# Optimization experiments

Measured on AMD Instinct MI355X. Metric: run time of the kernel, lower is better.

Reference implementation:

```python
import jax, jax.numpy as jnp
import numpy as np

# Rs_hidden = [(16,0),(16,1)] -> 16 scalar irreps (dim 1) then 16 vector irreps (dim 3)
B, N, M = 4, 80, 16
CH = M + 3 * M  # 64 channels
RADII = jnp.linspace(0.0, 1.0, 3)
GAMMA = 1.0 / (0.5 ** 2)  # gaussian rbf width = radii spacing
EPS = 1e-6

_lc = np.zeros((3, 3, 3), np.float32)
for i, j, k in [(0, 1, 2), (1, 2, 0), (2, 0, 1)]:
    _lc[i, j, k] = 1.0
    _lc[i, k, j] = -1.0
LC = jnp.asarray(_lc)  # Levi-Civita


def _si(t, w0, w1):
    """SelfInteraction: per-l mixing of multiplicities. t: [B, mi0 + 3*mi1, ...]."""
    mi0, mi1 = w0.shape[1], w1.shape[1]
    s = t[:, :mi0]
    v = t[:, mi0:].reshape(t.shape[0], mi1, 3, *t.shape[2:])
    os = jnp.einsum('om,nm...->no...', w0, s)
    ov = jnp.einsum('om,nmi...->noi...', w1, v)
    ov = ov.reshape(ov.shape[0], ov.shape[1] * 3, *ov.shape[3:])
    return jnp.concatenate([os, ov], axis=1)


def _norm_act(t, act):
    """NormActivation: scalar irreps -> act(x); vector irreps -> x * act(||x||)/||x||. Channel axis 1."""
    s = act(t[:, :M])
    v = t[:, M:].reshape(t.shape[0], M, 3, *t.shape[2:])
    n = jnp.sqrt(jnp.sum(v * v, axis=2, keepdims=True) + EPS)
    v = (v * act(n) / n).reshape(t.shape[0], 3 * M, *t.shape[2:])
    return jnp.concatenate([s, v], axis=1)


def _gate_mul(gate, target):
    """gate_normwise_multiply: multiply each irrep block of target by the L2 norm of the
    corresponding gate block (norm over the irrep components, channel axis 1)."""
    gs = jnp.abs(gate[:, :M])
    gv = gate[:, M:].reshape(gate.shape[0], M, 3, *gate.shape[2:])
    gn = jnp.sqrt(jnp.sum(gv * gv, axis=2) + EPS)
    factor = jnp.concatenate([gs, jnp.repeat(gn, 3, axis=1)], axis=1)
    return factor * target


def _interleave(a_t, b_t):
    """Interleave per-(m,l) blocks: [a_l0, b_l0, a_l1, b_l1] -> Rs_hidden_double layout."""
    return jnp.concatenate([a_t[:, :M], b_t[:, :M], a_t[:, M:], b_t[:, M:]], axis=1)


def _kernel(h_nei_diff, w_k00, w_k10, w_k01, w_k11):
    """SE3 point kernel for l in {0,1}, J<=2. Returns K[n,b,a,d,c] with d,c in irrep layout."""
    rad = jnp.sqrt(jnp.sum(h_nei_diff ** 2, axis=-1) + EPS)      # [B,N,N]
    nh = h_nei_diff / rad[..., None]                              # unit vectors
    rbf = jnp.exp(-GAMMA * (rad[..., None] - RADII) ** 2)        # [B,N,N,3]
    K00 = jnp.einsum('uvk,...k->...uv', w_k00, rbf)              # [B,N,N,M,M]
    K10 = jnp.einsum('uvk,...k,...i->...uiv', w_k10, rbf, nh).reshape(B, N, N, 3 * M, M)
    K01 = jnp.einsum('uvk,...k,...j->...uvj', w_k01, rbf, nh).reshape(B, N, N, M, 3 * M)
    RJ = jnp.einsum('juvk,...k->j...uv', w_k11, rbf)             # [3,B,N,N,M,M]
    eye = jnp.eye(3, dtype=rbf.dtype)
    cross = jnp.einsum('ijk,...k->...ij', LC, nh)                # J=1 basis
    outer = nh[..., :, None] * nh[..., None, :] - eye / 3.0      # J=2 basis
    base = (RJ[0][..., None, None] * eye
            + RJ[1][..., None, None] * cross[..., None, None, :, :]
            + RJ[2][..., None, None] * outer[..., None, None, :, :])  # [B,N,N,u,v,i,j]
    K11 = jnp.transpose(base, (0, 1, 2, 3, 5, 4, 6)).reshape(B, N, N, 3 * M, 3 * M)
    top = jnp.concatenate([K00, K01], axis=-1)
    bot = jnp.concatenate([K10, K11], axis=-1)
    return jnp.concatenate([top, bot], axis=-2)                  # [B,N,N,CH,CH]


def setup_inputs() -> dict:
    key = jax.random.key(0)
    ks = jax.random.split(key, 16)
    sc = 0.1
    d = {
        'x': jax.random.normal(ks[0], (B, CH, N), jnp.float32),
        'h_nei': jax.random.normal(ks[1], (B, CH, N), jnp.float32),
        'h_nei_diff': jax.random.normal(ks[2], (B, N, N, 3), jnp.float32),
        'mask': jax.random.uniform(ks[3], (B, N, N), jnp.float32),
        'w_k00': jax.random.normal(ks[4], (M, M, 3), jnp.float32) * sc,
        'w_k10': jax.random.normal(ks[5], (M, M, 3), jnp.float32) * sc,
        'w_k01': jax.random.normal(ks[6], (M, M, 3), jnp.float32) * sc,
        'w_k11': jax.random.normal(ks[7], (3, M, M, 3), jnp.float32) * sc,
        'si_z_w0': jax.random.normal(ks[8], (M, 2 * M), jnp.float32) * sc,
        'si_z_w1': jax.random.normal(ks[9], (M, 2 * M), jnp.float32) * sc,
        'si_r1_w0': jax.random.normal(ks[10], (M, M), jnp.float32) * sc,
        'si_r1_w1': jax.random.normal(ks[11], (M, M), jnp.float32) * sc,
        'si_r2_w0': jax.random.normal(ks[12], (M, M), jnp.float32) * sc,
        'si_r2_w1': jax.random.normal(ks[13], (M, M), jnp.float32) * sc,
        'si_ph_w0': jax.random.normal(ks[14], (M, 2 * M), jnp.float32) * sc,
        'si_ph_w1': jax.random.normal(ks[15], (M, 2 * M), jnp.float32) * sc,
    }
    return d


def reference(x, h_nei, h_nei_diff, mask, w_k00, w_k10, w_k01, w_k11,
              si_z_w0, si_z_w1, si_r1_w0, si_r1_w1, si_r2_w0, si_r2_w1,
              si_ph_w0, si_ph_w1):
    Kmat = _kernel(h_nei_diff, w_k00, w_k10, w_k01, w_k11)
    # masked neighbor conv: h_conv[n,d,b,a] = sum_c h_nei[n,c,a] K[n,b,a,d,c] mask[n,b,a]
    h_conv = jnp.einsum('nca,nbadc,nba->ndba', h_nei, Kmat, mask)
    sum_h = h_conv.sum(axis=-1)                                   # [B,CH,N]
    z = _norm_act(_si(_interleave(x, sum_h), si_z_w0, si_z_w1), jax.nn.sigmoid)
    r1 = _si(x, si_r1_w0, si_r1_w1)                               # [B,CH,N]
    r2 = _si(h_conv.reshape(B, CH, N * N), si_r2_w0, si_r2_w1).reshape(B, CH, N, N)
    r = _norm_act(r1[:, :, None, :] + r2, jax.nn.sigmoid)         # [B,CH,N,N]
    gated = _gate_mul(r, h_conv)
    sum_g = gated.sum(axis=-1)                                    # [B,CH,N]
    pre_h = _norm_act(_si(_interleave(x, sum_g), si_ph_w0, si_ph_w1), jnp.tanh)
    new_h = sum_h + _gate_mul(z, pre_h + sum_h)
    return new_h
```

## Files before the change

### kernel.cpp

```cpp
#include <hip/hip_runtime.h>
#include <math.h>

#define Bq 4
#define Nq 80
#define CHq 64
#define GAMMAq 4.0f
#define EPSq 1e-6f
#define PCWL 100
#define NQUAD 24


__global__ __launch_bounds__(64) void se3_precomp(
    const float* __restrict__ h_nei,
    const float* __restrict__ x,
    const float* __restrict__ w00,
    const float* __restrict__ w10,
    const float* __restrict__ w01,
    const float* __restrict__ w11,
    const float* __restrict__ wr10,
    const float* __restrict__ wr11,
    const float* __restrict__ wr20,
    const float* __restrict__ wr21,
    float* __restrict__ pc)
{
    const int na = blockIdx.x;
    const int n  = na / Nq, a = na - n * Nq;
    const int t  = threadIdx.x;
    const int u  = t & 15;
    const int kk = t >> 4;

    __shared__ float hsh[64];
    __shared__ float xsh[64];
    __shared__ float pout[16][PCWL];

    hsh[t] = h_nei[(size_t)n * CHq * Nq + t * Nq + a];
    xsh[t] = x    [(size_t)n * CHq * Nq + t * Nq + a];
    __syncthreads();

    if (kk < 3) {
        const int k = kk;
        float a00 = 0.f, a10 = 0.f;
        float c[3] = {0.f,0.f,0.f}, p0[3] = {0.f,0.f,0.f};
        float p1[3] = {0.f,0.f,0.f}, p2[3] = {0.f,0.f,0.f};
#pragma unroll
        for (int v = 0; v < 16; ++v) {
            const float s = hsh[v];
            a00 += w00[(u * 16 + v) * 3 + k] * s;
            a10 += w10[(u * 16 + v) * 3 + k] * s;
            const float w01v = w01[(u * 16 + v) * 3 + k];
            const float w110 = w11[((0 * 16 + u) * 16 + v) * 3 + k];
            const float w111 = w11[((1 * 16 + u) * 16 + v) * 3 + k];
            const float w112 = w11[((2 * 16 + u) * 16 + v) * 3 + k];
#pragma unroll
            for (int j = 0; j < 3; ++j) {
                const float Vj = hsh[16 + v * 3 + j];
                c[j]  += w01v * Vj;
                p0[j] += w110 * Vj;
                p1[j] += w111 * Vj;
                p2[j] += w112 * Vj;
            }
        }
        pout[u][0 + k] = a00;
        pout[u][3 + k] = a10;
#pragma unroll
        for (int j = 0; j < 3; ++j) {
            pout[u][6  + k * 3 + j] = c[j];
            pout[u][15 + k * 3 + j] = p0[j];
            pout[u][24 + k * 3 + j] = p1[j];
            pout[u][33 + k * 3 + j] = p2[j];
        }
    } else {
        float r1s = 0.f, r1v[3] = {0.f, 0.f, 0.f};
#pragma unroll
        for (int v = 0; v < 16; ++v) {
            r1s += wr10[u * 16 + v] * xsh[v];
            const float wv = wr11[u * 16 + v];
#pragma unroll
            for (int j = 0; j < 3; ++j) r1v[j] += wv * xsh[16 + v * 3 + j];
        }
        pout[u][42] = r1s;
#pragma unroll
        for (int j = 0; j < 3; ++j) pout[u][43 + j] = r1v[j];
        pout[u][46] = 0.f; pout[u][47] = 0.f;
#pragma unroll
        for (int j = 90; j < 96; ++j) pout[u][j] = 0.f;
    }
    __syncthreads();

    for (int c = kk; c < 42; c += 4) {
        const bool scalarType = (c < 3) || (c >= 6 && c < 15);
        const float* W = scalarType ? wr20 : wr21;
        float acc = 0.f;
#pragma unroll
        for (int v = 0; v < 16; ++v) acc += W[u * 16 + v] * pout[v][c];
        pout[u][48 + c] = acc;
    }
    __syncthreads();

    {
        float4* dst = reinterpret_cast<float4*>(pc) + (size_t)na * (NQUAD * 16) + u;
#pragma unroll
        for (int i = 0; i < 6; ++i) {
            const int c4 = kk + i * 4;
            dst[c4 * 16] = make_float4(pout[u][c4 * 4 + 0], pout[u][c4 * 4 + 1],
                                       pout[u][c4 * 4 + 2], pout[u][c4 * 4 + 3]);
        }
    }
}

__global__ __launch_bounds__(256) void se3_main(
    const float* __restrict__ x,
    const float* __restrict__ hdiff,
    const float* __restrict__ mask,
    const float* __restrict__ wz0,
    const float* __restrict__ wz1,
    const float* __restrict__ wp0,
    const float* __restrict__ wp1,
    const float* __restrict__ pc,
    float* __restrict__ out)
{
    const int nb    = blockIdx.x;
    const int n     = nb / Nq;
    const int bnode = nb - n * Nq;
    const int tid   = threadIdx.x;
    const int g     = tid >> 4;
    const int u     = tid & 15;

    __shared__ float wsh[4][512];
    __shared__ float redW[4][8][16];
    __shared__ float sumHs[64], sumGs[64];

#pragma unroll
    for (int i = 0; i < 2; ++i) {
        const int idx = tid + i * 256;
        wsh[0][idx] = wz0[idx];
        wsh[1][idx] = wz1[idx];
        wsh[2][idx] = wp0[idx];
        wsh[3][idx] = wp1[idx];
    }

    float shs = 0.f, shv0 = 0.f, shv1 = 0.f, shv2 = 0.f;
    float sgs = 0.f, sgv0 = 0.f, sgv1 = 0.f, sgv2 = 0.f;

    const float* drow = hdiff + (size_t)(n * Nq + bnode) * Nq * 3;
    const float* mrow = mask  + (size_t)(n * Nq + bnode) * Nq;
    const float third = 1.0f / 3.0f;

    for (int it = 0; it < 5; ++it) {
        const int a = it * 16 + g;

        const float d0 = drow[a * 3 + 0], d1 = drow[a * 3 + 1], d2 = drow[a * 3 + 2];
        const float m  = mrow[a];

        const float rad = sqrtf(d0 * d0 + d1 * d1 + d2 * d2 + EPSq);
        const float inv = 1.0f / rad;
        const float nh0 = d0 * inv, nh1 = d1 * inv, nh2 = d2 * inv;
        float rb[3];
        rb[0] = expf(-GAMMAq * rad * rad);
        { float t1 = rad - 0.5f; rb[1] = expf(-GAMMAq * t1 * t1); }
        { float t2 = rad - 1.0f; rb[2] = expf(-GAMMAq * t2 * t2); }

        const float4* p4 = reinterpret_cast<const float4*>(pc)
                         + (size_t)(n * Nq + a) * (NQUAD * 16) + u;

        float pa[48];
#pragma unroll
        for (int i = 0; i < 12; ++i)
            *reinterpret_cast<float4*>(&pa[i * 4]) = p4[i * 16];
        float pb[44];
#pragma unroll
        for (int i = 0; i < 11; ++i)
            *reinterpret_cast<float4*>(&pb[i * 4]) = p4[(12 + i) * 16];

        float as_ = 0.f, a10 = 0.f;
        float c01[3] = {0.f,0.f,0.f}, p0[3] = {0.f,0.f,0.f};
        float p1[3] = {0.f,0.f,0.f}, p2[3] = {0.f,0.f,0.f};
        float bs_ = 0.f, b10 = 0.f;
        float bc01[3] = {0.f,0.f,0.f}, bp0[3] = {0.f,0.f,0.f};
        float bp1[3] = {0.f,0.f,0.f}, bp2[3] = {0.f,0.f,0.f};
#pragma unroll
        for (int k = 0; k < 3; ++k) {
            const float r = rb[k];
            as_ += r * pa[0 + k];
            a10 += r * pa[3 + k];
            bs_ += r * pb[0 + k];
            b10 += r * pb[3 + k];
#pragma unroll
            for (int j = 0; j < 3; ++j) {
                c01[j]  += r * pa[6  + k * 3 + j];
                p0[j]   += r * pa[15 + k * 3 + j];
                p1[j]   += r * pa[24 + k * 3 + j];
                p2[j]   += r * pa[33 + k * 3 + j];
                bc01[j] += r * pb[6  + k * 3 + j];
                bp0[j]  += r * pb[15 + k * 3 + j];
                bp1[j]  += r * pb[24 + k * 3 + j];
                bp2[j]  += r * pb[33 + k * 3 + j];
            }
        }

        const float hcs = m * (as_ + c01[0] * nh0 + c01[1] * nh1 + c01[2] * nh2);
        const float cr0 = p1[1] * nh2 - p1[2] * nh1;
        const float cr1 = p1[2] * nh0 - p1[0] * nh2;
        const float cr2 = p1[0] * nh1 - p1[1] * nh0;
        const float pd  = p2[0] * nh0 + p2[1] * nh1 + p2[2] * nh2;
        const float hv0 = m * (nh0 * a10 + p0[0] + cr0 + nh0 * pd - p2[0] * third);
        const float hv1 = m * (nh1 * a10 + p0[1] + cr1 + nh1 * pd - p2[1] * third);
        const float hv2 = m * (nh2 * a10 + p0[2] + cr2 + nh2 * pd - p2[2] * third);

        const float r2s = m * (bs_ + bc01[0] * nh0 + bc01[1] * nh1 + bc01[2] * nh2);
        const float br0 = bp1[1] * nh2 - bp1[2] * nh1;
        const float br1 = bp1[2] * nh0 - bp1[0] * nh2;
        const float br2 = bp1[0] * nh1 - bp1[1] * nh0;
        const float bpd = bp2[0] * nh0 + bp2[1] * nh1 + bp2[2] * nh2;
        const float r2v0 = m * (nh0 * b10 + bp0[0] + br0 + nh0 * bpd - bp2[0] * third);
        const float r2v1 = m * (nh1 * b10 + bp0[1] + br1 + nh1 * bpd - bp2[1] * third);
        const float r2v2 = m * (nh2 * b10 + bp0[2] + br2 + nh2 * bpd - bp2[2] * third);

        const float r1s  = pa[42];
        const float r1v0 = pa[43], r1v1 = pa[44], r1v2 = pa[45];

        const float rs  = 1.0f / (1.0f + expf(-(r1s + r2s)));
        const float wv0 = r1v0 + r2v0, wv1 = r1v1 + r2v1, wv2 = r1v2 + r2v2;
        const float nn  = sqrtf(wv0 * wv0 + wv1 * wv1 + wv2 * wv2 + EPSq);
        const float sc  = (1.0f / (1.0f + expf(-nn))) / nn;
        const float rv0 = wv0 * sc, rv1 = wv1 * sc, rv2 = wv2 * sc;
        const float fs  = fabsf(rs);
        const float fv  = sqrtf(rv0 * rv0 + rv1 * rv1 + rv2 * rv2 + EPSq);

        shs += hcs;        shv0 += hv0;      shv1 += hv1;      shv2 += hv2;
        sgs += fs * hcs;   sgv0 += fv * hv0; sgv1 += fv * hv1; sgv2 += fv * hv2;
    }

    float vals[8] = {shs, shv0, shv1, shv2, sgs, sgv0, sgv1, sgv2};
#pragma unroll
    for (int q = 0; q < 8; ++q) {
        vals[q] += __shfl_xor(vals[q], 16, 64);
        vals[q] += __shfl_xor(vals[q], 32, 64);
    }
    const int wave = tid >> 6;
    if ((tid & 63) < 16) {
#pragma unroll
        for (int q = 0; q < 8; ++q) redW[wave][q][u] = vals[q];
    }
    __syncthreads();

    if (tid < 16) {
        float tacc[8];
#pragma unroll
        for (int q = 0; q < 8; ++q)
            tacc[q] = redW[0][q][tid] + redW[1][q][tid] + redW[2][q][tid] + redW[3][q][tid];
        sumHs[tid] = tacc[0];
        sumGs[tid] = tacc[4];
#pragma unroll
        for (int j = 0; j < 3; ++j) {
            sumHs[16 + tid * 3 + j] = tacc[1 + j];
            sumGs[16 + tid * 3 + j] = tacc[5 + j];
        }
    }
    __syncthreads();

    if (tid < 16) {
        const float* xb = x + (size_t)n * CHq * Nq + bnode;

        float zs_in = 0.f, ps_in = 0.f;
        float zv[3] = {0.f, 0.f, 0.f};
        float pv[3] = {0.f, 0.f, 0.f};
#pragma unroll
        for (int mm = 0; mm < 32; ++mm) {
            float Sh, Sg;
            if (mm < 16) { const float xv = xb[mm * Nq]; Sh = xv; Sg = xv; }
            else         { Sh = sumHs[mm - 16]; Sg = sumGs[mm - 16]; }
            zs_in += wsh[0][tid * 32 + mm] * Sh;
            ps_in += wsh[2][tid * 32 + mm] * Sg;
            const float wz = wsh[1][tid * 32 + mm];
            const float wp = wsh[3][tid * 32 + mm];
#pragma unroll
            for (int j = 0; j < 3; ++j) {
                float Vh, Vg;
                if (mm < 16) { const float xv = xb[(16 + mm * 3 + j) * Nq]; Vh = xv; Vg = xv; }
                else { Vh = sumHs[16 + (mm - 16) * 3 + j]; Vg = sumGs[16 + (mm - 16) * 3 + j]; }
                zv[j] += wz * Vh;
                pv[j] += wp * Vg;
            }
        }

        const float zs  = 1.0f / (1.0f + expf(-zs_in));
        const float zn  = sqrtf(zv[0] * zv[0] + zv[1] * zv[1] + zv[2] * zv[2] + EPSq);
        const float zsc = (1.0f / (1.0f + expf(-zn))) / zn;
        const float zv0 = zv[0] * zsc, zv1 = zv[1] * zsc, zv2 = zv[2] * zsc;
        const float phs = tanhf(ps_in);
        const float pn  = sqrtf(pv[0] * pv[0] + pv[1] * pv[1] + pv[2] * pv[2] + EPSq);
        const float psc = tanhf(pn) / pn;
        const float pv0 = pv[0] * psc, pv1 = pv[1] * psc, pv2 = pv[2] * psc;
        const float gfs = fabsf(zs);
        const float gfv = sqrtf(zv0 * zv0 + zv1 * zv1 + zv2 * zv2 + EPSq);

        float* ob = out + (size_t)n * CHq * Nq + bnode;
        const float sh_s = sumHs[tid];
        ob[tid * Nq] = sh_s + gfs * (phs + sh_s);
#pragma unroll
        for (int j = 0; j < 3; ++j) {
            const float shv = sumHs[16 + tid * 3 + j];
            const float pvj = (j == 0) ? pv0 : ((j == 1) ? pv1 : pv2);
            ob[(16 + tid * 3 + j) * Nq] = shv + gfv * (pvj + shv);
        }
    }
}

extern "C" void kernel_launch(void* const* d_in, const int* in_sizes, int n_in,
                              void* d_out, int out_size, void* d_ws, size_t ws_size,
                              hipStream_t stream) {
    const float* x      = (const float*)d_in[0];
    const float* h_nei  = (const float*)d_in[1];
    const float* hdiff  = (const float*)d_in[2];
    const float* mask   = (const float*)d_in[3];
    const float* w00    = (const float*)d_in[4];
    const float* w10    = (const float*)d_in[5];
    const float* w01    = (const float*)d_in[6];
    const float* w11    = (const float*)d_in[7];
    const float* wz0    = (const float*)d_in[8];
    const float* wz1    = (const float*)d_in[9];
    const float* wr10   = (const float*)d_in[10];
    const float* wr11   = (const float*)d_in[11];
    const float* wr20   = (const float*)d_in[12];
    const float* wr21   = (const float*)d_in[13];
    const float* wp0    = (const float*)d_in[14];
    const float* wp1    = (const float*)d_in[15];
    float* out = (float*)d_out;
    float* pc  = (float*)d_ws;

    se3_precomp<<<Bq * Nq, 64, 0, stream>>>(
        h_nei, x, w00, w10, w01, w11, wr10, wr11, wr20, wr21, pc);
    se3_main<<<Bq * Nq, 256, 0, stream>>>(
        x, hdiff, mask, wz0, wz1, wp0, wp1, pc, out);
}
```

Baseline: 27.69 us.

## Split precompute reductions across more threads, remap block indices, use fast exp

The precompute kernel grows from 64 to 192 threads. Each v-reduction is split into two halves whose partial sums are combined in shared memory, and the second-stage r2 mixing is spread over 96 threads instead of 64. Both kernels remap blockIdx so that consecutive blocks alternate across batch and node halves, likely to spread work across XCDs and their caches. expf is replaced by __expf in the main kernel, trading a little accuracy for cheaper transcendentals.

```diff
diff --git a/kernel.cpp b/kernel.cpp
--- a/kernel.cpp
+++ b/kernel.cpp
@@ -10,7 +10,7 @@
 #define NQUAD 24
 
 
-__global__ __launch_bounds__(64) void se3_precomp(
+__global__ __launch_bounds__(192) void se3_precomp(
     const float* __restrict__ h_nei,
     const float* __restrict__ x,
     const float* __restrict__ w00,
@@ -23,87 +23,121 @@
     const float* __restrict__ wr21,
     float* __restrict__ pc)
 {
-    const int na = blockIdx.x;
-    const int n  = na / Nq, a = na - n * Nq;
-    const int t  = threadIdx.x;
-    const int u  = t & 15;
-    const int kk = t >> 4;
+    const int L   = blockIdx.x & 7;
+    const int idx = blockIdx.x >> 3;
+    const int n   = L >> 1;
+    const int a   = (L & 1) * 40 + idx;
+    const int na  = n * Nq + a;
+    const int tid = threadIdx.x;
 
     __shared__ float hsh[64];
     __shared__ float xsh[64];
+    __shared__ float psh[2][42][16];
+    __shared__ float r1sh[2][4][16];
     __shared__ float pout[16][PCWL];
 
-    hsh[t] = h_nei[(size_t)n * CHq * Nq + t * Nq + a];
-    xsh[t] = x    [(size_t)n * CHq * Nq + t * Nq + a];
-    __syncthreads();
-
-    if (kk < 3) {
-        const int k = kk;
-        float a00 = 0.f, a10 = 0.f;
-        float c[3] = {0.f,0.f,0.f}, p0[3] = {0.f,0.f,0.f};
-        float p1[3] = {0.f,0.f,0.f}, p2[3] = {0.f,0.f,0.f};
-#pragma unroll
-        for (int v = 0; v < 16; ++v) {
-            const float s = hsh[v];
-            a00 += w00[(u * 16 + v) * 3 + k] * s;
-            a10 += w10[(u * 16 + v) * 3 + k] * s;
-            const float w01v = w01[(u * 16 + v) * 3 + k];
-            const float w110 = w11[((0 * 16 + u) * 16 + v) * 3 + k];
-            const float w111 = w11[((1 * 16 + u) * 16 + v) * 3 + k];
-            const float w112 = w11[((2 * 16 + u) * 16 + v) * 3 + k];
+    if (tid < 64)       hsh[tid]      = h_nei[(size_t)n * CHq * Nq + tid * Nq + a];
+    else if (tid < 128) xsh[tid - 64] = x    [(size_t)n * CHq * Nq + (tid - 64) * Nq + a];
+    __syncthreads();
+
+    if (tid < 128) {
+        const int u    = tid & 15;
+        const int q    = tid >> 4;
+        const int half = q & 1;
+        const int kk   = q >> 1;
+        const int v0   = half * 8;
+
+        if (kk < 3) {
+            const int k = kk;
+            float a00 = 0.f, a10 = 0.f;
+            float c[3] = {0.f,0.f,0.f}, p0[3] = {0.f,0.f,0.f};
+            float p1[3] = {0.f,0.f,0.f}, p2[3] = {0.f,0.f,0.f};
+#pragma unroll
+            for (int i = 0; i < 8; ++i) {
+                const int v = v0 + i;
+                const float s = hsh[v];
+                a00 += w00[(u * 16 + v) * 3 + k] * s;
+                a10 += w10[(u * 16 + v) * 3 + k] * s;
+                const float w01v = w01[(u * 16 + v) * 3 + k];
+                const float w110 = w11[((0 * 16 + u) * 16 + v) * 3 + k];
+                const float w111 = w11[((1 * 16 + u) * 16 + v) * 3 + k];
+                const float w112 = w11[((2 * 16 + u) * 16 + v) * 3 + k];
+#pragma unroll
+                for (int j = 0; j < 3; ++j) {
+                    const float Vj = hsh[16 + v * 3 + j];
+                    c[j]  += w01v * Vj;
+                    p0[j] += w110 * Vj;
+                    p1[j] += w111 * Vj;
+                    p2[j] += w112 * Vj;
+                }
+            }
+            psh[half][0 + k][u] = a00;
+            psh[half][3 + k][u] = a10;
 #pragma unroll
             for (int j = 0; j < 3; ++j) {
-                const float Vj = hsh[16 + v * 3 + j];
-                c[j]  += w01v * Vj;
-                p0[j] += w110 * Vj;
-                p1[j] += w111 * Vj;
-                p2[j] += w112 * Vj;
-            }
-        }
-        pout[u][0 + k] = a00;
-        pout[u][3 + k] = a10;
-#pragma unroll
-        for (int j = 0; j < 3; ++j) {
-            pout[u][6  + k * 3 + j] = c[j];
-            pout[u][15 + k * 3 + j] = p0[j];
-            pout[u][24 + k * 3 + j] = p1[j];
-            pout[u][33 + k * 3 + j] = p2[j];
-        }
-    } else {
-        float r1s = 0.f, r1v[3] = {0.f, 0.f, 0.f};
-#pragma unroll
-        for (int v = 0; v < 16; ++v) {
-            r1s += wr10[u * 16 + v] * xsh[v];
-            const float wv = wr11[u * 16 + v];
-#pragma unroll
-            for (int j = 0; j < 3; ++j) r1v[j] += wv * xsh[16 + v * 3 + j];
-        }
-        pout[u][42] = r1s;
-#pragma unroll
-        for (int j = 0; j < 3; ++j) pout[u][43 + j] = r1v[j];
-        pout[u][46] = 0.f; pout[u][47] = 0.f;
-#pragma unroll
-        for (int j = 90; j < 96; ++j) pout[u][j] = 0.f;
-    }
-    __syncthreads();
-
-    for (int c = kk; c < 42; c += 4) {
-        const bool scalarType = (c < 3) || (c >= 6 && c < 15);
-        const float* W = scalarType ? wr20 : wr21;
-        float acc = 0.f;
-#pragma unroll
-        for (int v = 0; v < 16; ++v) acc += W[u * 16 + v] * pout[v][c];
-        pout[u][48 + c] = acc;
+                psh[half][6  + k * 3 + j][u] = c[j];
+                psh[half][15 + k * 3 + j][u] = p0[j];
+                psh[half][24 + k * 3 + j][u] = p1[j];
+                psh[half][33 + k * 3 + j][u] = p2[j];
+            }
+        } else {
+            float r1s = 0.f, r1v[3] = {0.f, 0.f, 0.f};
+#pragma unroll
+            for (int i = 0; i < 8; ++i) {
+                const int v = v0 + i;
+                r1s += wr10[u * 16 + v] * xsh[v];
+                const float wv = wr11[u * 16 + v];
+#pragma unroll
+                for (int j = 0; j < 3; ++j) r1v[j] += wv * xsh[16 + v * 3 + j];
+            }
+            r1sh[half][0][u] = r1s;
+#pragma unroll
+            for (int j = 0; j < 3; ++j) r1sh[half][1 + j][u] = r1v[j];
+        }
+    }
+    __syncthreads();
+
+    if (tid < 96) {
+        const int u  = tid & 15;
+        const int kk = tid >> 4;
+#pragma unroll
+        for (int c = kk * 7; c < kk * 7 + 7; ++c)
+            pout[u][c] = psh[0][c][u] + psh[1][c][u];
+        if (kk == 0) {
+#pragma unroll
+            for (int j = 0; j < 4; ++j)
+                pout[u][42 + j] = r1sh[0][j][u] + r1sh[1][j][u];
+            pout[u][46] = 0.f; pout[u][47] = 0.f;
+#pragma unroll
+            for (int j = 90; j < 96; ++j) pout[u][j] = 0.f;
+        }
+    }
+    __syncthreads();
+
+    if (tid < 96) {
+        const int u  = tid & 15;
+        const int kk = tid >> 4;
+#pragma unroll
+        for (int c = kk * 7; c < kk * 7 + 7; ++c) {
+            const bool scalarType = (c < 3) || (c >= 6 && c < 15);
+            const float* W = scalarType ? wr20 : wr21;
+            float acc = 0.f;
+#pragma unroll
+            for (int v = 0; v < 16; ++v) acc += W[u * 16 + v] * pout[v][c];
+            pout[u][48 + c] = acc;
+        }
     }
     __syncthreads();
 
     {
-        float4* dst = reinterpret_cast<float4*>(pc) + (size_t)na * (NQUAD * 16) + u;
-#pragma unroll
-        for (int i = 0; i < 6; ++i) {
-            const int c4 = kk + i * 4;
-            dst[c4 * 16] = make_float4(pout[u][c4 * 4 + 0], pout[u][c4 * 4 + 1],
-                                       pout[u][c4 * 4 + 2], pout[u][c4 * 4 + 3]);
+        float4* dst = reinterpret_cast<float4*>(pc) + (size_t)na * (NQUAD * 16);
+#pragma unroll
+        for (int i = 0; i < 2; ++i) {
+            const int qi = tid + i * 192;
+            const int c4 = qi >> 4;
+            const int u  = qi & 15;
+            dst[c4 * 16 + u] = make_float4(pout[u][c4 * 4 + 0], pout[u][c4 * 4 + 1],
+                                           pout[u][c4 * 4 + 2], pout[u][c4 * 4 + 3]);
         }
     }
 }
@@ -119,9 +153,10 @@
     const float* __restrict__ pc,
     float* __restrict__ out)
 {
-    const int nb    = blockIdx.x;
-    const int n     = nb / Nq;
-    const int bnode = nb - n * Nq;
+    const int L     = blockIdx.x & 7;
+    const int idx   = blockIdx.x >> 3;
+    const int n     = L >> 1;
+    const int bnode = (L & 1) * 40 + idx;
     const int tid   = threadIdx.x;
     const int g     = tid >> 4;
     const int u     = tid & 15;
@@ -132,11 +167,11 @@
 
 #pragma unroll
     for (int i = 0; i < 2; ++i) {
-        const int idx = tid + i * 256;
-        wsh[0][idx] = wz0[idx];
-        wsh[1][idx] = wz1[idx];
-        wsh[2][idx] = wp0[idx];
-        wsh[3][idx] = wp1[idx];
+        const int widx = tid + i * 256;
+        wsh[0][widx] = wz0[widx];
+        wsh[1][widx] = wz1[widx];
+        wsh[2][widx] = wp0[widx];
+        wsh[3][widx] = wp1[widx];
     }
 
     float shs = 0.f, shv0 = 0.f, shv1 = 0.f, shv2 = 0.f;
@@ -156,9 +191,9 @@
         const float inv = 1.0f / rad;
         const float nh0 = d0 * inv, nh1 = d1 * inv, nh2 = d2 * inv;
         float rb[3];
-        rb[0] = expf(-GAMMAq * rad * rad);
-        { float t1 = rad - 0.5f; rb[1] = expf(-GAMMAq * t1 * t1); }
-        { float t2 = rad - 1.0f; rb[2] = expf(-GAMMAq * t2 * t2); }
+        rb[0] = __expf(-GAMMAq * rad * rad);
+        { float t1 = rad - 0.5f; rb[1] = __expf(-GAMMAq * t1 * t1); }
+        { float t2 = rad - 1.0f; rb[2] = __expf(-GAMMAq * t2 * t2); }
 
         const float4* p4 = reinterpret_cast<const float4*>(pc)
                          + (size_t)(n * Nq + a) * (NQUAD * 16) + u;
@@ -219,10 +254,10 @@
         const float r1s  = pa[42];
         const float r1v0 = pa[43], r1v1 = pa[44], r1v2 = pa[45];
 
-        const float rs  = 1.0f / (1.0f + expf(-(r1s + r2s)));
+        const float rs  = 1.0f / (1.0f + __expf(-(r1s + r2s)));
         const float wv0 = r1v0 + r2v0, wv1 = r1v1 + r2v1, wv2 = r1v2 + r2v2;
         const float nn  = sqrtf(wv0 * wv0 + wv1 * wv1 + wv2 * wv2 + EPSq);
-        const float sc  = (1.0f / (1.0f + expf(-nn))) / nn;
+        const float sc  = (1.0f / (1.0f + __expf(-nn))) / nn;
         const float rv0 = wv0 * sc, rv1 = wv1 * sc, rv2 = wv2 * sc;
         const float fs  = fabsf(rs);
         const float fv  = sqrtf(rv0 * rv0 + rv1 * rv1 + rv2 * rv2 + EPSq);
@@ -284,9 +319,9 @@
             }
         }
 
-        const float zs  = 1.0f / (1.0f + expf(-zs_in));
+        const float zs  = 1.0f / (1.0f + __expf(-zs_in));
         const float zn  = sqrtf(zv[0] * zv[0] + zv[1] * zv[1] + zv[2] * zv[2] + EPSq);
-        const float zsc = (1.0f / (1.0f + expf(-zn))) / zn;
+        const float zsc = (1.0f / (1.0f + __expf(-zn))) / zn;
         const float zv0 = zv[0] * zsc, zv1 = zv[1] * zsc, zv2 = zv[2] * zsc;
         const float phs = tanhf(ps_in);
         const float pn  = sqrtf(pv[0] * pv[0] + pv[1] * pv[1] + pv[2] * pv[2] + EPSq);
@@ -329,7 +364,7 @@
     float* out = (float*)d_out;
     float* pc  = (float*)d_ws;
 
-    se3_precomp<<<Bq * Nq, 64, 0, stream>>>(
+    se3_precomp<<<Bq * Nq, 192, 0, stream>>>(
         h_nei, x, w00, w10, w01, w11, wr10, wr11, wr20, wr21, pc);
     se3_main<<<Bq * Nq, 256, 0, stream>>>(
         x, hdiff, mask, wz0, wz1, wp0, wp1, pc, out);
```

Result: faster. 24.86 us (-10.2%).
